# Kernel tuning notes

Measured on AMD Instinct MI355X. Metric: run time of the kernel, lower is better.

Reference implementation:

```python
import jax, jax.numpy as jnp
import numpy as np
from math import sqrt

B, LQ, LK = 4, 256, 50000
EDGE_IN, NODE_IN, OUT = 128, 128, 256
KV_IN = NODE_IN + EDGE_IN  # 256


def setup_inputs() -> dict:
    key = jax.random.key(0)
    ks = jax.random.split(key, 8)
    s = 0.05
    return {
        "query": jax.random.normal(ks[0], (B, LQ, EDGE_IN), jnp.float32),
        "input": jax.random.normal(ks[1], (B, LK, KV_IN), jnp.float32),
        "Wq": jax.random.normal(ks[2], (OUT, EDGE_IN), jnp.float32) * s,
        "bq": jax.random.normal(ks[3], (OUT,), jnp.float32) * s,
        "Wk": jax.random.normal(ks[4], (OUT, KV_IN), jnp.float32) * s,
        "bk": jax.random.normal(ks[5], (OUT,), jnp.float32) * s,
        "Wv": jax.random.normal(ks[6], (OUT, KV_IN), jnp.float32) * s,
        "bv": jax.random.normal(ks[7], (OUT,), jnp.float32) * s,
    }


def reference(query, input, Wq, bq, Wk, bk, Wv, bv):
    norm = 1.0 / sqrt(OUT)
    Q = query @ Wq.T + bq            # [B, LQ, OUT]
    K = input @ Wk.T + bk            # [B, LK, OUT]
    V = input @ Wv.T + bv            # [B, LK, OUT]
    alpha = jnp.einsum("bqd,bkd->bqk", Q, K) * norm  # [B, LQ, LK]
    alpha = jax.nn.softmax(alpha, axis=-1)
    # z = alpha^T * V broadcasts only because LQ == OUT:
    # out[b, j] = sum_k alpha[b, j, k] * V[b, k, j]
    return jnp.einsum("bqk,bkq->bq", alpha, V)      # [B, OUT]
```

## Files before the change

kernel.cpp:

```cpp
#include <hip/hip_runtime.h>
#include <hip/hip_bf16.h>
#include <stdint.h>

using f32x4  = __attribute__((ext_vector_type(4))) float;
using bf16x8 = __attribute__((ext_vector_type(8))) short;

constexpr int BATCH = 4;
constexpr int LQ_   = 256;
constexpr int LK_   = 50000;
constexpr int OUTD  = 256;
constexpr int EIN   = 128;
constexpr int TR    = 16;
constexpr int NT    = LK_ / TR;
constexpr int KCH   = 64;

__device__ __forceinline__ uint32_t f2bf(float f) {
  uint32_t u = __builtin_bit_cast(uint32_t, f);
  u = (u + 0x7fffu + ((u >> 16) & 1u)) >> 16;
  return u;
}
__device__ __forceinline__ uint32_t cvtpk(float lo, float hi) {
  uint32_t r;
  asm volatile("v_cvt_pk_bf16_f32 %0, %1, %2" : "=v"(r) : "v"(lo), "v"(hi));
  return r;
}

__device__ __forceinline__ void block_sync_lds() {
  asm volatile("s_waitcnt lgkmcnt(0)" ::: "memory");
  __builtin_amdgcn_sched_barrier(0);
  __builtin_amdgcn_s_barrier();
  __builtin_amdgcn_sched_barrier(0);
}

__global__ __launch_bounds__(256) void prep_all(
    const float* __restrict__ query, const float* __restrict__ Wq,
    const float* __restrict__ bq,    const float* __restrict__ Wk,
    const float* __restrict__ Wv,    ushort* __restrict__ Gn,
    ushort* __restrict__ Wvbf,       float* __restrict__ numden)
{
  const int blk = blockIdx.x, tid = threadIdx.x;
  if (blk >= 64) {
    if (blk < 96) {
      int base = (blk - 64) * 2048 + tid * 8;
      float4 a = *(const float4*)(Wv + base);
      float4 c = *(const float4*)(Wv + base + 4);
      uint4 pk;
      pk.x = f2bf(a.x) | (f2bf(a.y) << 16);
      pk.y = f2bf(a.z) | (f2bf(a.w) << 16);
      pk.z = f2bf(c.x) | (f2bf(c.y) << 16);
      pk.w = f2bf(c.z) | (f2bf(c.w) << 16);
      *(uint4*)(Wvbf + base) = pk;
    } else {
      for (int i = tid; i < 2 * BATCH * OUTD; i += 256) numden[i] = 0.f;
    }
    return;
  }
  __shared__ float qin[16 * EIN];
  __shared__ float Qr [16 * OUTD];
  const int b = blk >> 4, q0 = (blk & 15) * 16;
  {
    int idx = tid * 8;
    int row = idx >> 7, c = idx & 127;
    const float* p = query + ((size_t)b * LQ_ + q0 + row) * EIN + c;
    float4 a = *(const float4*)p;
    float4 d = *(const float4*)(p + 4);
    float* q = &qin[row * EIN + c];
    q[0]=a.x; q[1]=a.y; q[2]=a.z; q[3]=a.w; q[4]=d.x; q[5]=d.y; q[6]=d.z; q[7]=d.w;
  }
  __syncthreads();

  float acc[16];
  {
    float bias = bq[tid];
#pragma unroll
    for (int i = 0; i < 16; ++i) acc[i] = bias;
  }
  for (int d4 = 0; d4 < EIN / 4; ++d4) {
    f32x4 w4 = *(const f32x4*)(Wq + tid * EIN + d4 * 4);
#pragma unroll
    for (int i = 0; i < 16; ++i) {
      f32x4 q4 = *(const f32x4*)(qin + i * EIN + d4 * 4);
      acc[i] += q4[0]*w4[0] + q4[1]*w4[1] + q4[2]*w4[2] + q4[3]*w4[3];
    }
  }
#pragma unroll
  for (int i = 0; i < 16; ++i) Qr[i * OUTD + tid] = acc[i];
  __syncthreads();

  float acc2[16];
#pragma unroll
  for (int i = 0; i < 16; ++i) acc2[i] = 0.f;
  for (int d4 = 0; d4 < OUTD / 4; ++d4) {
    float w0 = Wk[(d4*4+0) * OUTD + tid];
    float w1 = Wk[(d4*4+1) * OUTD + tid];
    float w2 = Wk[(d4*4+2) * OUTD + tid];
    float w3 = Wk[(d4*4+3) * OUTD + tid];
#pragma unroll
    for (int i = 0; i < 16; ++i) {
      f32x4 q4 = *(const f32x4*)(Qr + i * OUTD + d4 * 4);
      acc2[i] += q4[0]*w0 + q4[1]*w1 + q4[2]*w2 + q4[3]*w3;
    }
  }
  const float norm = 0.0625f;
#pragma unroll
  for (int i = 0; i < 16; ++i)
    Gn[((size_t)b * LQ_ + q0 + i) * OUTD + tid] = (ushort)f2bf(acc2[i] * norm);
}

__global__ __launch_bounds__(512, 4) void attn_main(
    const float*  __restrict__ input, const ushort* __restrict__ Gn,
    const ushort* __restrict__ Wvbf,  float* __restrict__ num,
    float* __restrict__ den)
{
  __shared__ ushort in_lds[2 * 4096];
  const int idx = blockIdx.x;
  const int b = idx >> 7, qb = (idx >> 6) & 1, kch = idx & (KCH - 1);
  const int t0 = (kch * NT) >> 6, t1 = ((kch + 1) * NT) >> 6;
  const int tid = threadIdx.x, w = tid >> 6, l = tid & 63;
  const int lg = l >> 4, lr = l & 15;
  const float* src = input + (size_t)b * LK_ * 256;

  const int arow = qb * 128 + w * 16 + lr;
  const ushort* gp = Gn   + ((size_t)b * LQ_ + arow) * 256 + lg * 8;
  const ushort* vp = Wvbf + (size_t)arow * 256 + lg * 8;
  bf16x8 ga[8], wa[8];
#pragma unroll
  for (int k = 0; k < 8; ++k) {
    ga[k] = *(const bf16x8*)(gp + k * 32);
    wa[k] = *(const bf16x8*)(vp + k * 32);
    asm volatile("" : "+v"(ga[k]), "+v"(wa[k]));
  }

  float numr[4], denr[4];
#pragma unroll
  for (int r = 0; r < 4; ++r) { numr[r] = 0.f; denr[r] = 0.f; }

  const int srow = tid >> 5, sfbg = tid & 31;
  const float* sbase = src + sfbg * 8;
  float4 s0, s1;
  auto loadreg = [&](int t) {
    int row = t * TR + srow;
    row = row < LK_ ? row : LK_ - 1;
    const float* p = sbase + (size_t)row * 256;
    s0 = *(const float4*)p;
    s1 = *(const float4*)(p + 4);
  };
  auto writebuf = [&](int buf) {
    char* base = (char*)in_lds + buf * 8192;
    uint4 pk;
    pk.x = cvtpk(s0.x, s0.y);
    pk.y = cvtpk(s0.z, s0.w);
    pk.z = cvtpk(s1.x, s1.y);
    pk.w = cvtpk(s1.z, s1.w);
    *(uint4*)(base + sfbg * 256 + ((srow ^ (sfbg & 15)) << 4)) = pk;
  };

  loadreg(t0);
  writebuf(t0 & 1);
  loadreg(t0 + 1);
  block_sync_lds();

  for (int t = t0; t < t1; ++t) {
    const char* bbuf = (const char*)in_lds + (t & 1) * 8192;
    f32x4 aS = {0,0,0,0};
    f32x4 aV = {0,0,0,0};
#pragma unroll
    for (int ks = 0; ks < 8; ++ks) {
      const int fb = ks * 4 + lg;
      bf16x8 bb = *(const bf16x8*)(bbuf + fb * 256 + ((lr ^ (fb & 15)) << 4));
      aS = __builtin_amdgcn_mfma_f32_16x16x32_bf16(ga[ks], bb, aS, 0, 0, 0);
      aV = __builtin_amdgcn_mfma_f32_16x16x32_bf16(wa[ks], bb, aV, 0, 0, 0);
    }
#pragma unroll
    for (int r = 0; r < 4; ++r) {
      float e = __expf(aS[r]);
      denr[r] += e;
      numr[r] += e * aV[r];
    }
    if (t + 1 < t1) {
      writebuf((t + 1) & 1);
      if (t + 2 < t1) loadreg(t + 2);
    }
    block_sync_lds();
  }

#pragma unroll
  for (int r = 0; r < 4; ++r) {
    float d_ = denr[r], n_ = numr[r];
#pragma unroll
    for (int m = 1; m < 16; m <<= 1) {
      d_ += __shfl_xor(d_, m, 64);
      n_ += __shfl_xor(n_, m, 64);
    }
    if (lr == 0) {
      int q = qb * 128 + w * 16 + lg * 4 + r;
      atomicAdd(&den[b * OUTD + q], d_);
      atomicAdd(&num[b * OUTD + q], n_);
    }
  }
}

__global__ __launch_bounds__(256) void finalize(const float* __restrict__ num,
                                                const float* __restrict__ den,
                                                const float* __restrict__ bv,
                                                float* __restrict__ out) {
  int i = blockIdx.x * 256 + threadIdx.x;
  out[i] = num[i] / den[i] + bv[i & 255];
}

extern "C" void kernel_launch(void* const* d_in, const int* in_sizes, int n_in,
                              void* d_out, int out_size, void* d_ws, size_t ws_size,
                              hipStream_t stream)
{
  const float* query = (const float*)d_in[0];
  const float* input = (const float*)d_in[1];
  const float* Wq    = (const float*)d_in[2];
  const float* bq    = (const float*)d_in[3];
  const float* Wk    = (const float*)d_in[4];
  const float* Wv    = (const float*)d_in[6];
  const float* bv    = (const float*)d_in[7];
  float* out = (float*)d_out;

  char* ws = (char*)d_ws;
  ushort* Gn     = (ushort*)ws;
  ushort* Wvbf   = (ushort*)(ws + 524288);
  float*  numden = (float*)(ws + 524288 + 131072);
  float*  num    = numden;
  float*  den    = numden + BATCH * OUTD;

  prep_all<<<97, 256, 0, stream>>>(query, Wq, bq, Wk, Wv, Gn, Wvbf, numden);
  attn_main<<<BATCH * 2 * KCH, 512, 0, stream>>>(input, Gn, Wvbf, num, den);
  finalize<<<BATCH, 256, 0, stream>>>(num, den, bv, out);
}
```

Baseline: 109.4 us.

## Share input tiles across all query rows with 1024-thread blocks and 32-row tiles

Merges the two query-half blocks into one 1024-thread block covering all 256 query rows, so each input key tile is loaded from global memory and converted to bf16 once instead of twice. The key tile grows from 16 to 32 rows and is processed as two 16-row MFMA sub-tiles. The LDS swizzle is reworked for 512-byte rows using precomputed read pointers, and out-of-range tail rows are masked. The aim is to roughly halve HBM traffic on the dominant input stream. In exchange, blocks are larger with 16 waves sharing each barrier, and register pressure under the 1024-thread launch bound is higher.

```diff
diff --git a/kernel.cpp b/kernel.cpp
--- a/kernel.cpp
+++ b/kernel.cpp
@@ -10,8 +10,9 @@
 constexpr int LK_   = 50000;
 constexpr int OUTD  = 256;
 constexpr int EIN   = 128;
-constexpr int TR    = 16;
+constexpr int TR    = 32;
 constexpr int NT    = LK_ / TR;
+constexpr int NTC   = (LK_ + TR - 1) / TR;
 constexpr int KCH   = 64;
 
 __device__ __forceinline__ uint32_t f2bf(float f) {
@@ -107,20 +108,20 @@
     Gn[((size_t)b * LQ_ + q0 + i) * OUTD + tid] = (ushort)f2bf(acc2[i] * norm);
 }
 
-__global__ __launch_bounds__(512, 4) void attn_main(
+__global__ __launch_bounds__(1024, 4) void attn_main(
     const float*  __restrict__ input, const ushort* __restrict__ Gn,
     const ushort* __restrict__ Wvbf,  float* __restrict__ num,
     float* __restrict__ den)
 {
-  __shared__ ushort in_lds[2 * 4096];
+  __shared__ ushort in_lds[2 * 8192];
   const int idx = blockIdx.x;
-  const int b = idx >> 7, qb = (idx >> 6) & 1, kch = idx & (KCH - 1);
-  const int t0 = (kch * NT) >> 6, t1 = ((kch + 1) * NT) >> 6;
+  const int b = idx >> 6, kch = idx & (KCH - 1);
+  const int t0 = (kch * NTC) >> 6, t1 = ((kch + 1) * NTC) >> 6;
   const int tid = threadIdx.x, w = tid >> 6, l = tid & 63;
   const int lg = l >> 4, lr = l & 15;
   const float* src = input + (size_t)b * LK_ * 256;
 
-  const int arow = qb * 128 + w * 16 + lr;
+  const int arow = w * 16 + lr;
   const ushort* gp = Gn   + ((size_t)b * LQ_ + arow) * 256 + lg * 8;
   const ushort* vp = Wvbf + (size_t)arow * 256 + lg * 8;
   bf16x8 ga[8], wa[8];
@@ -134,6 +135,17 @@
   float numr[4], denr[4];
 #pragma unroll
   for (int r = 0; r < 4; ++r) { numr[r] = 0.f; denr[r] = 0.f; }
+
+  const char* rp[8];
+#pragma unroll
+  for (int ks = 0; ks < 8; ++ks) {
+    const int fb = ks * 4 + lg;
+    const int slot0 = lr ^ fb;
+    const int slotmin = slot0 & ~16;
+    rp[ks] = (const char*)in_lds + fb * 512 + (slotmin << 4);
+  }
+  const int hi16 = ((lg >= 4) ? 1 : 0);
+  (void)hi16;
 
   const int srow = tid >> 5, sfbg = tid & 31;
   const float* sbase = src + sfbg * 8;
@@ -145,14 +157,15 @@
     s0 = *(const float4*)p;
     s1 = *(const float4*)(p + 4);
   };
+  const int swoff = sfbg * 512 + ((srow ^ sfbg) << 4);
   auto writebuf = [&](int buf) {
-    char* base = (char*)in_lds + buf * 8192;
+    char* base = (char*)in_lds + buf * 16384;
     uint4 pk;
     pk.x = cvtpk(s0.x, s0.y);
     pk.y = cvtpk(s0.z, s0.w);
     pk.z = cvtpk(s1.x, s1.y);
     pk.w = cvtpk(s1.z, s1.w);
-    *(uint4*)(base + sfbg * 256 + ((srow ^ (sfbg & 15)) << 4)) = pk;
+    *(uint4*)(base + swoff) = pk;
   };
 
   loadreg(t0);
@@ -160,22 +173,27 @@
   loadreg(t0 + 1);
   block_sync_lds();
 
+  const bool tail = (t1 == NTC);
   for (int t = t0; t < t1; ++t) {
-    const char* bbuf = (const char*)in_lds + (t & 1) * 8192;
-    f32x4 aS = {0,0,0,0};
-    f32x4 aV = {0,0,0,0};
-#pragma unroll
-    for (int ks = 0; ks < 8; ++ks) {
-      const int fb = ks * 4 + lg;
-      bf16x8 bb = *(const bf16x8*)(bbuf + fb * 256 + ((lr ^ (fb & 15)) << 4));
-      aS = __builtin_amdgcn_mfma_f32_16x16x32_bf16(ga[ks], bb, aS, 0, 0, 0);
-      aV = __builtin_amdgcn_mfma_f32_16x16x32_bf16(wa[ks], bb, aV, 0, 0, 0);
-    }
-#pragma unroll
-    for (int r = 0; r < 4; ++r) {
-      float e = __expf(aS[r]);
-      denr[r] += e;
-      numr[r] += e * aV[r];
+    const int bufoff = (t & 1) * 16384;
+#pragma unroll
+    for (int nt = 0; nt < 2; ++nt) {
+      f32x4 aS = {0,0,0,0};
+      f32x4 aV = {0,0,0,0};
+#pragma unroll
+      for (int ks = 0; ks < 8; ++ks) {
+        const int off = bufoff + (((ks < 4) ? nt : 1 - nt) << 8);
+        bf16x8 bb = *(const bf16x8*)(rp[ks] + off);
+        aS = __builtin_amdgcn_mfma_f32_16x16x32_bf16(ga[ks], bb, aS, 0, 0, 0);
+        aV = __builtin_amdgcn_mfma_f32_16x16x32_bf16(wa[ks], bb, aV, 0, 0, 0);
+      }
+      const bool valid = !tail || (t * TR + nt * 16 + lr) < LK_;
+#pragma unroll
+      for (int r = 0; r < 4; ++r) {
+        float e = valid ? __expf(aS[r]) : 0.f;
+        denr[r] += e;
+        numr[r] += e * aV[r];
+      }
     }
     if (t + 1 < t1) {
       writebuf((t + 1) & 1);
@@ -193,7 +211,7 @@
       n_ += __shfl_xor(n_, m, 64);
     }
     if (lr == 0) {
-      int q = qb * 128 + w * 16 + lg * 4 + r;
+      int q = w * 16 + lg * 4 + r;
       atomicAdd(&den[b * OUTD + q], d_);
       atomicAdd(&num[b * OUTD + q], n_);
     }
@@ -229,6 +247,6 @@
   float*  den    = numden + BATCH * OUTD;
 
   prep_all<<<97, 256, 0, stream>>>(query, Wq, bq, Wk, Wv, Gn, Wvbf, numden);
-  attn_main<<<BATCH * 2 * KCH, 512, 0, stream>>>(input, Gn, Wvbf, num, den);
+  attn_main<<<BATCH * KCH, 1024, 0, stream>>>(input, Gn, Wvbf, num, den);
   finalize<<<BATCH, 256, 0, stream>>>(num, den, bv, out);
 }
```

New measurement: 107.9 us. Within noise of the previous version (-1.4%).
